# Kernel optimization log

Hardware: AMD Instinct MI355X
Metric: run time of the kernel (lower is better)

Reference implementation:

```python
import jax, jax.numpy as jnp
import numpy as np

NUM_USER = 100000
NUM_ITEM = 50000
N = NUM_USER + NUM_ITEM
E = 1200000
D = 64          # emb_size
F_ITEM = 384    # raw item multimodal feature dim
K = 3           # number of global embedding rows (summed over dim 0)
N_LAYERS = 4
EPS = 1e-8      # F.cosine_similarity default eps


def setup_inputs() -> dict:
    key = jax.random.key(0)
    ks = jax.random.split(key, 9)
    return {
        "adj_row": jax.random.randint(ks[0], (E,), 0, N),
        "adj_col": jax.random.randint(ks[1], (E,), 0, N),
        # scaled like a degree-normalized adjacency (avg degree ~8)
        "adj_val": jax.random.uniform(ks[2], (E,), jnp.float32) / 8.0,
        "user_fea": jax.random.normal(ks[3], (NUM_USER, D), jnp.float32) * 0.1,
        "item_fea": jax.random.normal(ks[4], (NUM_ITEM, F_ITEM), jnp.float32) * 0.1,
        "g_emb_u": jax.random.normal(ks[5], (K, D), jnp.float32) * 0.1,
        "g_emb_i": jax.random.normal(ks[6], (K, D), jnp.float32) * 0.1,
        "mlp_w": jax.random.normal(ks[7], (D, F_ITEM), jnp.float32) * (1.0 / np.sqrt(F_ITEM)),
        "mlp_b": jnp.zeros((D,), jnp.float32),
    }


def _cosine_sim(a, b):
    # matches F.cosine_similarity(a, b, dim=-1) with eps clamp on norms
    na = jnp.maximum(jnp.linalg.norm(a, axis=-1), EPS)
    nb = jnp.maximum(jnp.linalg.norm(b, axis=-1), EPS)
    return jnp.sum(a * b, axis=-1) / (na * nb)


def reference(adj_row, adj_col, adj_val, user_fea, item_fea, g_emb_u, g_emb_i, mlp_w, mlp_b):
    # global embeddings summed over modality dim
    user_emb = user_fea + jnp.sum(g_emb_u, axis=0)                       # [U, D]
    item_emb = jnp.tanh(item_fea @ mlp_w.T + mlp_b) + jnp.sum(g_emb_i, axis=0)  # [I, D]
    ego = jnp.concatenate([user_emb, item_emb], axis=0)                  # [N, D]

    x = ego
    acc = ego  # sum over layers, includes layer-0 (ego) term
    for _ in range(N_LAYERS):
        # sparse adj @ x as gather -> scale -> segment-sum scatter
        x = jax.ops.segment_sum(adj_val[:, None] * x[adj_col], adj_row, num_segments=N)
        w = _cosine_sim(x, ego)     # [N]
        x = w[:, None] * x          # einsum('a,ab->ab')
        acc = acc + x

    return acc[:NUM_USER], acc[NUM_USER:]
```

## Files before the change

kernel.cpp:

```cpp
#include <hip/hip_runtime.h>
#include <hip/hip_bf16.h>

#define U_NUM 100000
#define I_NUM 50000
#define N_NUM 150000
#define E_NUM 1200000
#define D 64
#define F_IT 384
#define CAP 32
#define EPSV 1e-8f
#define FXS 524288.0f
#define FXI (1.0f / 524288.0f)

#define NBIN 586
#define RPB 256
#define FBLK 586
#define CELL_CAP 16
#define OV_CAP 64

typedef unsigned short ushort_t;
typedef unsigned int uint_t;
typedef short bf16x8 __attribute__((ext_vector_type(8)));
typedef float f32x4 __attribute__((ext_vector_type(4)));

__device__ __forceinline__ ushort_t f2bf(float f) {
    uint_t x = __float_as_uint(f);
    uint_t r = x + 0x7fffu + ((x >> 16) & 1u);
    return (ushort_t)(r >> 16);
}
__device__ __forceinline__ float bfu2f(uint_t u_lo16) {
    return __uint_as_float(u_lo16 << 16);
}
__device__ __forceinline__ void dec8(uint4 u, float* f) {
    f[0] = bfu2f(u.x & 0xffffu); f[1] = bfu2f(u.x >> 16);
    f[2] = bfu2f(u.y & 0xffffu); f[3] = bfu2f(u.y >> 16);
    f[4] = bfu2f(u.z & 0xffffu); f[5] = bfu2f(u.z >> 16);
    f[6] = bfu2f(u.w & 0xffffu); f[7] = bfu2f(u.w >> 16);
}

__global__ void k_prep(const float* __restrict__ w, const float* __restrict__ gu,
                       const float* __restrict__ gi,
                       short* __restrict__ wbf, float* __restrict__ gsu,
                       float* __restrict__ gsi, int* __restrict__ ovcnt) {
    int b = blockIdx.x, t = threadIdx.x;
    if (b < 96) {
        int i = b * 256 + t;
        wbf[i] = (short)f2bf(w[i]);
    } else {
        if (t < 64) gsu[t] = gu[t] + gu[64 + t] + gu[128 + t];
        else if (t < 128) { int d = t - 64; gsi[d] = gi[d] + gi[64 + d] + gi[128 + d]; }
        for (int i = t; i < NBIN; i += 256) ovcnt[i] = 0;
    }
}

#define ITEM_B 782
#define USER_B 1563

__global__ __launch_bounds__(256) void k_mega(
        const int* __restrict__ row, const int* __restrict__ col,
        const float* __restrict__ val,
        const float* __restrict__ ufea, const float* __restrict__ ifea,
        const float* __restrict__ bvec,
        const short* __restrict__ wbf,
        const float* __restrict__ gsu, const float* __restrict__ gsi,
        int2* __restrict__ cellbuf, int* __restrict__ cellcnt,
        int* __restrict__ ovcnt, int2* __restrict__ ovbuf,
        float* __restrict__ ego, ushort_t* __restrict__ egob) {
    __shared__ int bincnt[NBIN];
    int b = blockIdx.x;
    int grp = b / 9, slot = b % 9;
    int tid = threadIdx.x;

    if (slot < 2) {
        int fid = grp * 2 + slot;
        if (fid >= FBLK) return;
        for (int i = tid; i < NBIN; i += 256) bincnt[i] = 0;
        __syncthreads();
        int t = fid * 256 + tid;
        if (t < E_NUM / 8) {
#pragma unroll
            for (int k = 0; k < 8; k++) {
                int e = k * (E_NUM / 8) + t;
                int r = row[e], c = col[e];
                float v = val[e];
                int bn = r >> 8;
                int key = c | ((r & 255) << 18);
                int ls = atomicAdd(&bincnt[bn], 1);
                if (ls < CELL_CAP) {
                    cellbuf[((size_t)fid * NBIN + bn) * CELL_CAP + ls] =
                        make_int2(key, __float_as_int(v));
                } else {
                    int o = atomicAdd(&ovcnt[bn], 1);
                    if (o < OV_CAP) ovbuf[bn * OV_CAP + o] = make_int2(key, __float_as_int(v));
                }
            }
        }
        __syncthreads();
        for (int i = tid; i < NBIN; i += 256)
            cellcnt[(size_t)fid * NBIN + i] = min(bincnt[i], CELL_CAP);
    } else if (slot < 4) {
        int iid = grp * 2 + (slot - 2);
        if (iid >= ITEM_B) return;
        int wave = tid >> 6, lane = tid & 63;
        int q = lane >> 4, m = lane & 15;
        int ibase = iid * 64 + wave * 16;
        int irow = min(ibase + m, I_NUM - 1);
        const float* arow = ifea + (size_t)irow * F_IT + q * 8;

        f32x4 av[4];
#pragma unroll
        for (int n = 0; n < 4; n++) av[n] = (f32x4){0.f, 0.f, 0.f, 0.f};
        float4 nfa0 = ((const float4*)(arow))[0];
        float4 nfa1 = ((const float4*)(arow))[1];
#pragma unroll
        for (int c = 0; c < 12; c++) {
            float4 fa0 = nfa0, fa1 = nfa1;
            if (c < 11) {
                nfa0 = ((const float4*)(arow + (c + 1) * 32))[0];
                nfa1 = ((const float4*)(arow + (c + 1) * 32))[1];
            }
            bf16x8 af;
            af[0] = (short)f2bf(fa0.x); af[1] = (short)f2bf(fa0.y);
            af[2] = (short)f2bf(fa0.z); af[3] = (short)f2bf(fa0.w);
            af[4] = (short)f2bf(fa1.x); af[5] = (short)f2bf(fa1.y);
            af[6] = (short)f2bf(fa1.z); af[7] = (short)f2bf(fa1.w);
#pragma unroll
            for (int n = 0; n < 4; n++) {
                bf16x8 bf = *(const bf16x8*)(wbf + (size_t)(n * 16 + m) * F_IT + c * 32 + q * 8);
                av[n] = __builtin_amdgcn_mfma_f32_16x16x32_bf16(af, bf, av[n], 0, 0, 0);
            }
        }
#pragma unroll
        for (int n = 0; n < 4; n++) {
            int dim = n * 16 + m;
            float bb = bvec[dim];
            float gg = gsi[dim];
#pragma unroll
            for (int rr = 0; rr < 4; rr++) {
                int item = ibase + q * 4 + rr;
                if (item < I_NUM) {
                    float v = tanhf(av[n][rr] + bb) + gg;
                    size_t o = (size_t)(U_NUM + item) * D + dim;
                    ego[o] = v;
                    egob[o] = f2bf(v);
                }
            }
        }
    } else {
        int uid = grp * 5 + (slot - 4);
        if (uid >= USER_B) return;
        int t = uid * 256 + tid;
        size_t base = (size_t)t * 16;
        if (base >= (size_t)U_NUM * D) return;
        int d0 = (int)(base & 63);
        float f[16];
#pragma unroll
        for (int k = 0; k < 4; k++) {
            float4 v = ((const float4*)(ufea + base))[k];
            f[4 * k] = v.x; f[4 * k + 1] = v.y; f[4 * k + 2] = v.z; f[4 * k + 3] = v.w;
        }
#pragma unroll
        for (int j = 0; j < 16; j++) f[j] += gsu[d0 + j];
#pragma unroll
        for (int k = 0; k < 4; k++) {
            ((float4*)(ego + base))[k] = make_float4(f[4 * k], f[4 * k + 1], f[4 * k + 2], f[4 * k + 3]);
        }
        uint4 u0, u1;
        u0.x = (uint_t)f2bf(f[0]) | ((uint_t)f2bf(f[1]) << 16);
        u0.y = (uint_t)f2bf(f[2]) | ((uint_t)f2bf(f[3]) << 16);
        u0.z = (uint_t)f2bf(f[4]) | ((uint_t)f2bf(f[5]) << 16);
        u0.w = (uint_t)f2bf(f[6]) | ((uint_t)f2bf(f[7]) << 16);
        u1.x = (uint_t)f2bf(f[8]) | ((uint_t)f2bf(f[9]) << 16);
        u1.y = (uint_t)f2bf(f[10]) | ((uint_t)f2bf(f[11]) << 16);
        u1.z = (uint_t)f2bf(f[12]) | ((uint_t)f2bf(f[13]) << 16);
        u1.w = (uint_t)f2bf(f[14]) | ((uint_t)f2bf(f[15]) << 16);
        ((uint4*)(egob + base))[0] = u0;
        ((uint4*)(egob + base))[1] = u1;
    }
}

__global__ __launch_bounds__(256) void k_bucket(const int2* __restrict__ cellbuf,
                                                const int* __restrict__ cellcnt,
                                                const int* __restrict__ ovcnt,
                                                const int2* __restrict__ ovbuf,
                                                int* __restrict__ cnt,
                                                int2* __restrict__ bkt) {
    __shared__ int lc[RPB];
    int bn = blockIdx.x, tid = threadIdx.x;
    lc[tid] = 0;
    __syncthreads();
    int rbase = bn << 8;
    int f0 = tid, f1 = tid + 256, f2 = tid + 512;
    int c0 = cellcnt[(size_t)f0 * NBIN + bn];
    int c1 = cellcnt[(size_t)f1 * NBIN + bn];
    int c2 = (f2 < FBLK) ? cellcnt[(size_t)f2 * NBIN + bn] : 0;
#pragma unroll
    for (int h = 0; h < 3; h++) {
        int f = (h == 0) ? f0 : ((h == 1) ? f1 : f2);
        int c = (h == 0) ? c0 : ((h == 1) ? c1 : c2);
        const int2* cp = cellbuf + ((size_t)f * NBIN + bn) * CELL_CAP;
        for (int i = 0; i < c; i++) {
            int2 e = cp[i];
            int rl = e.x >> 18;
            int s = atomicAdd(&lc[rl], 1);
            if (s < CAP) bkt[(size_t)(rbase + rl) * CAP + s] = make_int2(e.x & 0x3ffff, e.y);
        }
    }
    int oc = min(ovcnt[bn], OV_CAP);
    for (int i = tid; i < oc; i += 256) {
        int2 e = ovbuf[bn * OV_CAP + i];
        int rl = e.x >> 18;
        int s = atomicAdd(&lc[rl], 1);
        if (s < CAP) bkt[(size_t)(rbase + rl) * CAP + s] = make_int2(e.x & 0x3ffff, e.y);
    }
    __syncthreads();
    int r = rbase + tid;
    if (r < N_NUM) cnt[r] = lc[tid];
}

#define ACC8(A, VS, X) \
    A[0] += __float2int_rn(VS * bfu2f(X.x & 0xffffu)); A[1] += __float2int_rn(VS * bfu2f(X.x >> 16)); \
    A[2] += __float2int_rn(VS * bfu2f(X.y & 0xffffu)); A[3] += __float2int_rn(VS * bfu2f(X.y >> 16)); \
    A[4] += __float2int_rn(VS * bfu2f(X.z & 0xffffu)); A[5] += __float2int_rn(VS * bfu2f(X.z >> 16)); \
    A[6] += __float2int_rn(VS * bfu2f(X.w & 0xffffu)); A[7] += __float2int_rn(VS * bfu2f(X.w >> 16));

__device__ __forceinline__ float row_weight(const float* a, const float* e) {
    float dot = 0.f, nx = 0.f, ne = 0.f;
#pragma unroll
    for (int j = 0; j < 8; j++) {
        dot += a[j] * e[j]; nx += a[j] * a[j]; ne += e[j] * e[j];
    }
#pragma unroll
    for (int m = 1; m < 8; m <<= 1) {
        dot += __shfl_xor(dot, m);
        nx  += __shfl_xor(nx, m);
        ne  += __shfl_xor(ne, m);
    }
    return dot / (fmaxf(sqrtf(nx), EPSV) * fmaxf(sqrtf(ne), EPSV));
}

__device__ __forceinline__ void gather_row(const ushort_t* __restrict__ xb,
                                           const int2* __restrict__ bp, int deg, int l,
                                           int* __restrict__ a) {
#pragma unroll
    for (int j = 0; j < 8; j++) a[j] = 0;
#pragma unroll
    for (int k = 0; k < 4; k++) {
        if (k * 8 < deg) {
            int2 pc = bp[l + k * 8];
            float vs[8];
            uint4 xu[8];
#pragma unroll
            for (int j = 0; j < 8; j++) {
                int cc = __shfl(pc.x, j, 8);
                float v = __int_as_float(__shfl(pc.y, j, 8));
                if ((k * 8 + j) >= deg) { cc = 0; v = 0.f; }
                vs[j] = v * FXS;
                xu[j] = ((const uint4*)xb)[(size_t)cc * 8 + l];
            }
#pragma unroll
            for (int j = 0; j < 8; j++) { ACC8(a, vs[j], xu[j]); }
        }
    }
}

__global__ __launch_bounds__(256) void k_spmm(const ushort_t* __restrict__ xb,
                                              const ushort_t* __restrict__ egob,
                                              const int* __restrict__ cnt,
                                              const int2* __restrict__ bkt,
                                              ushort_t* __restrict__ xob) {
    int t = blockIdx.x * 256 + threadIdx.x;
    int l = t & 7, r = t >> 3;
    if (r >= N_NUM) return;
    int deg = min(cnt[r], CAP);
    int a[8];
    gather_row(xb, bkt + (size_t)r * CAP, deg, l, a);
    float af[8];
#pragma unroll
    for (int j = 0; j < 8; j++) af[j] = (float)a[j] * FXI;
    float e[8]; dec8(((const uint4*)egob)[(size_t)r * 8 + l], e);
    float wgt = row_weight(af, e);
    uint4 ov;
    ov.x = (uint_t)f2bf(wgt * af[0]) | ((uint_t)f2bf(wgt * af[1]) << 16);
    ov.y = (uint_t)f2bf(wgt * af[2]) | ((uint_t)f2bf(wgt * af[3]) << 16);
    ov.z = (uint_t)f2bf(wgt * af[4]) | ((uint_t)f2bf(wgt * af[5]) << 16);
    ov.w = (uint_t)f2bf(wgt * af[6]) | ((uint_t)f2bf(wgt * af[7]) << 16);
    ((uint4*)xob)[(size_t)r * 8 + l] = ov;
}

__global__ __launch_bounds__(256) void k_spmm4(const ushort_t* __restrict__ x3,
                                               const ushort_t* __restrict__ x1,
                                               const ushort_t* __restrict__ x2,
                                               const float* __restrict__ ego,
                                               const int* __restrict__ cnt,
                                               const int2* __restrict__ bkt,
                                               float* __restrict__ out) {
    int t = blockIdx.x * 256 + threadIdx.x;
    int l = t & 7, r = t >> 3;
    if (r >= N_NUM) return;
    int deg = min(cnt[r], CAP);
    int a[8];
    gather_row(x3, bkt + (size_t)r * CAP, deg, l, a);
    float af[8];
#pragma unroll
    for (int j = 0; j < 8; j++) af[j] = (float)a[j] * FXI;
    size_t rb = (size_t)r * D + l * 8;
    float e[8];
    float4 e0 = ((const float4*)(ego + rb))[0];
    float4 e1 = ((const float4*)(ego + rb))[1];
    e[0] = e0.x; e[1] = e0.y; e[2] = e0.z; e[3] = e0.w;
    e[4] = e1.x; e[5] = e1.y; e[6] = e1.z; e[7] = e1.w;
    float wgt = row_weight(af, e);
    float x1d[8], x2d[8], x3d[8];
    dec8(((const uint4*)x1)[(size_t)r * 8 + l], x1d);
    dec8(((const uint4*)x2)[(size_t)r * 8 + l], x2d);
    dec8(((const uint4*)x3)[(size_t)r * 8 + l], x3d);
    float s[8];
#pragma unroll
    for (int j = 0; j < 8; j++) s[j] = e[j] + x1d[j] + x2d[j] + x3d[j] + wgt * af[j];
    ((float4*)(out + rb))[0] = make_float4(s[0], s[1], s[2], s[3]);
    ((float4*)(out + rb))[1] = make_float4(s[4], s[5], s[6], s[7]);
}

extern "C" void kernel_launch(void* const* d_in, const int* in_sizes, int n_in,
                              void* d_out, int out_size, void* d_ws, size_t ws_size,
                              hipStream_t stream) {
    const int*   adj_row  = (const int*)d_in[0];
    const int*   adj_col  = (const int*)d_in[1];
    const float* adj_val  = (const float*)d_in[2];
    const float* user_fea = (const float*)d_in[3];
    const float* item_fea = (const float*)d_in[4];
    const float* gu       = (const float*)d_in[5];
    const float* gi       = (const float*)d_in[6];
    const float* mlp_w    = (const float*)d_in[7];
    const float* mlp_b    = (const float*)d_in[8];

    float* out = (float*)d_out;

    char* ws = (char*)d_ws;
    size_t off = 0;
    float*    ego  = (float*)(ws + off);    off += (size_t)N_NUM * D * 4;
    ushort_t* egob = (ushort_t*)(ws + off); off += (size_t)N_NUM * D * 2;
    size_t x1off = off;
    ushort_t* x1   = (ushort_t*)(ws + off); off += (size_t)N_NUM * D * 2;
    ushort_t* x2   = (ushort_t*)(ws + off); off += (size_t)N_NUM * D * 2;
    ushort_t* x3   = (ushort_t*)(ws + off); off += (size_t)N_NUM * D * 2;
    int*      cnt  = (int*)(ws + off);      off += (size_t)N_NUM * 4;
    short*    wbf  = (short*)(ws + off);    off += (size_t)D * F_IT * 2;
    float*    gsu  = (float*)(ws + off);    off += 64 * 4;
    float*    gsi  = (float*)(ws + off);    off += 64 * 4;
    off = (off + 255) & ~(size_t)255;
    int2*     bkt  = (int2*)(ws + off);     off += (size_t)N_NUM * CAP * 8;
    int*      cellcnt = (int*)(ws + off);   off += (size_t)FBLK * NBIN * 4;
    int*      ovcnt   = (int*)(ws + off);   off += (size_t)NBIN * 4;
    int2*     ovbuf   = (int2*)(ws + off);  off += (size_t)NBIN * OV_CAP * 8;
    int2*     cellbuf = (int2*)(ws + x1off);

    k_prep<<<97, 256, 0, stream>>>(mlp_w, gu, gi, wbf, gsu, gsi, ovcnt);
    k_mega<<<391 * 9, 256, 0, stream>>>(adj_row, adj_col, adj_val, user_fea, item_fea,
                                        mlp_b, wbf, gsu, gsi,
                                        cellbuf, cellcnt, ovcnt, ovbuf, ego, egob);
    k_bucket<<<NBIN, 256, 0, stream>>>(cellbuf, cellcnt, ovcnt, ovbuf, cnt, bkt);
    int g = ((size_t)N_NUM * 8 + 255) / 256;
    k_spmm<<<g, 256, 0, stream>>>(egob, egob, cnt, bkt, x1);
    k_spmm<<<g, 256, 0, stream>>>(x1,   egob, cnt, bkt, x2);
    k_spmm<<<g, 256, 0, stream>>>(x2,   egob, cnt, bkt, x3);
    k_spmm4<<<g, 256, 0, stream>>>(x3, x1, x2, ego, cnt, bkt, out);
}
```

Before: 412.1 us.

## Split mega kernel, use SoA padded adjacency buckets with vector loads

Splits the fused multi-role kernel into separate edge-fill, item-MLP and user-embedding kernels, and doubles the number of fill blocks while halving per-cell capacity. The bucket kernel now writes column indices and values as separate arrays and pads each row to a multiple of 8 with zero entries. The SpMM gather can then read 8 neighbors with int4/float4 loads instead of shuffling, and the SpMM kernels gain occupancy hints. Padding adds wasted gathers of row 0. The smaller cell capacity may push more edges into the bounded overflow buffer, which risks dropping edges if it fills.

New measurement: 442.7 us. +7.4%, slower.

```diff
diff --git a/kernel.cpp b/kernel.cpp
--- a/kernel.cpp
+++ b/kernel.cpp
@@ -14,8 +14,8 @@
 
 #define NBIN 586
 #define RPB 256
-#define FBLK 586
-#define CELL_CAP 16
+#define FBLK 1172
+#define CELL_CAP 8
 #define OV_CAP 64
 
 typedef unsigned short ushort_t;
@@ -53,130 +53,128 @@
     }
 }
 
-#define ITEM_B 782
-#define USER_B 1563
-
-__global__ __launch_bounds__(256) void k_mega(
+__global__ __launch_bounds__(256) void k_fill(
         const int* __restrict__ row, const int* __restrict__ col,
         const float* __restrict__ val,
-        const float* __restrict__ ufea, const float* __restrict__ ifea,
-        const float* __restrict__ bvec,
-        const short* __restrict__ wbf,
-        const float* __restrict__ gsu, const float* __restrict__ gsi,
         int2* __restrict__ cellbuf, int* __restrict__ cellcnt,
-        int* __restrict__ ovcnt, int2* __restrict__ ovbuf,
+        int* __restrict__ ovcnt, int2* __restrict__ ovbuf) {
+    __shared__ int bincnt[NBIN];
+    int fid = blockIdx.x, tid = threadIdx.x;
+    for (int i = tid; i < NBIN; i += 256) bincnt[i] = 0;
+    __syncthreads();
+    int t = fid * 256 + tid;
+    if (t < E_NUM / 4) {
+        int r[4], c[4];
+        float v[4];
+#pragma unroll
+        for (int k = 0; k < 4; k++) {
+            int e = k * (E_NUM / 4) + t;
+            r[k] = row[e]; c[k] = col[e]; v[k] = val[e];
+        }
+#pragma unroll
+        for (int k = 0; k < 4; k++) {
+            int bn = r[k] >> 8;
+            int key = c[k] | ((r[k] & 255) << 18);
+            int ls = atomicAdd(&bincnt[bn], 1);
+            if (ls < CELL_CAP) {
+                cellbuf[((size_t)fid * NBIN + bn) * CELL_CAP + ls] =
+                    make_int2(key, __float_as_int(v[k]));
+            } else {
+                int o = atomicAdd(&ovcnt[bn], 1);
+                if (o < OV_CAP) ovbuf[bn * OV_CAP + o] = make_int2(key, __float_as_int(v[k]));
+            }
+        }
+    }
+    __syncthreads();
+    for (int i = tid; i < NBIN; i += 256)
+        cellcnt[(size_t)fid * NBIN + i] = min(bincnt[i], CELL_CAP);
+}
+
+#define ITEM_B 782
+__global__ __launch_bounds__(256) void k_item(
+        const float* __restrict__ ifea, const float* __restrict__ bvec,
+        const short* __restrict__ wbf, const float* __restrict__ gsi,
         float* __restrict__ ego, ushort_t* __restrict__ egob) {
-    __shared__ int bincnt[NBIN];
-    int b = blockIdx.x;
-    int grp = b / 9, slot = b % 9;
+    int iid = blockIdx.x;
     int tid = threadIdx.x;
-
-    if (slot < 2) {
-        int fid = grp * 2 + slot;
-        if (fid >= FBLK) return;
-        for (int i = tid; i < NBIN; i += 256) bincnt[i] = 0;
-        __syncthreads();
-        int t = fid * 256 + tid;
-        if (t < E_NUM / 8) {
-#pragma unroll
-            for (int k = 0; k < 8; k++) {
-                int e = k * (E_NUM / 8) + t;
-                int r = row[e], c = col[e];
-                float v = val[e];
-                int bn = r >> 8;
-                int key = c | ((r & 255) << 18);
-                int ls = atomicAdd(&bincnt[bn], 1);
-                if (ls < CELL_CAP) {
-                    cellbuf[((size_t)fid * NBIN + bn) * CELL_CAP + ls] =
-                        make_int2(key, __float_as_int(v));
-                } else {
-                    int o = atomicAdd(&ovcnt[bn], 1);
-                    if (o < OV_CAP) ovbuf[bn * OV_CAP + o] = make_int2(key, __float_as_int(v));
-                }
+    int wave = tid >> 6, lane = tid & 63;
+    int q = lane >> 4, m = lane & 15;
+    int ibase = iid * 64 + wave * 16;
+    int irow = min(ibase + m, I_NUM - 1);
+    const float* arow = ifea + (size_t)irow * F_IT + q * 8;
+
+    f32x4 av[4];
+#pragma unroll
+    for (int n = 0; n < 4; n++) av[n] = (f32x4){0.f, 0.f, 0.f, 0.f};
+    float4 nfa0 = ((const float4*)(arow))[0];
+    float4 nfa1 = ((const float4*)(arow))[1];
+#pragma unroll
+    for (int c = 0; c < 12; c++) {
+        float4 fa0 = nfa0, fa1 = nfa1;
+        if (c < 11) {
+            nfa0 = ((const float4*)(arow + (c + 1) * 32))[0];
+            nfa1 = ((const float4*)(arow + (c + 1) * 32))[1];
+        }
+        bf16x8 af;
+        af[0] = (short)f2bf(fa0.x); af[1] = (short)f2bf(fa0.y);
+        af[2] = (short)f2bf(fa0.z); af[3] = (short)f2bf(fa0.w);
+        af[4] = (short)f2bf(fa1.x); af[5] = (short)f2bf(fa1.y);
+        af[6] = (short)f2bf(fa1.z); af[7] = (short)f2bf(fa1.w);
+#pragma unroll
+        for (int n = 0; n < 4; n++) {
+            bf16x8 bf = *(const bf16x8*)(wbf + (size_t)(n * 16 + m) * F_IT + c * 32 + q * 8);
+            av[n] = __builtin_amdgcn_mfma_f32_16x16x32_bf16(af, bf, av[n], 0, 0, 0);
+        }
+    }
+#pragma unroll
+    for (int n = 0; n < 4; n++) {
+        int dim = n * 16 + m;
+        float bb = bvec[dim];
+        float gg = gsi[dim];
+#pragma unroll
+        for (int rr = 0; rr < 4; rr++) {
+            int item = ibase + q * 4 + rr;
+            if (item < I_NUM) {
+                float v = tanhf(av[n][rr] + bb) + gg;
+                size_t o = (size_t)(U_NUM + item) * D + dim;
+                ego[o] = v;
+                egob[o] = f2bf(v);
             }
         }
-        __syncthreads();
-        for (int i = tid; i < NBIN; i += 256)
-            cellcnt[(size_t)fid * NBIN + i] = min(bincnt[i], CELL_CAP);
-    } else if (slot < 4) {
-        int iid = grp * 2 + (slot - 2);
-        if (iid >= ITEM_B) return;
-        int wave = tid >> 6, lane = tid & 63;
-        int q = lane >> 4, m = lane & 15;
-        int ibase = iid * 64 + wave * 16;
-        int irow = min(ibase + m, I_NUM - 1);
-        const float* arow = ifea + (size_t)irow * F_IT + q * 8;
-
-        f32x4 av[4];
-#pragma unroll
-        for (int n = 0; n < 4; n++) av[n] = (f32x4){0.f, 0.f, 0.f, 0.f};
-        float4 nfa0 = ((const float4*)(arow))[0];
-        float4 nfa1 = ((const float4*)(arow))[1];
-#pragma unroll
-        for (int c = 0; c < 12; c++) {
-            float4 fa0 = nfa0, fa1 = nfa1;
-            if (c < 11) {
-                nfa0 = ((const float4*)(arow + (c + 1) * 32))[0];
-                nfa1 = ((const float4*)(arow + (c + 1) * 32))[1];
-            }
-            bf16x8 af;
-            af[0] = (short)f2bf(fa0.x); af[1] = (short)f2bf(fa0.y);
-            af[2] = (short)f2bf(fa0.z); af[3] = (short)f2bf(fa0.w);
-            af[4] = (short)f2bf(fa1.x); af[5] = (short)f2bf(fa1.y);
-            af[6] = (short)f2bf(fa1.z); af[7] = (short)f2bf(fa1.w);
-#pragma unroll
-            for (int n = 0; n < 4; n++) {
-                bf16x8 bf = *(const bf16x8*)(wbf + (size_t)(n * 16 + m) * F_IT + c * 32 + q * 8);
-                av[n] = __builtin_amdgcn_mfma_f32_16x16x32_bf16(af, bf, av[n], 0, 0, 0);
-            }
-        }
-#pragma unroll
-        for (int n = 0; n < 4; n++) {
-            int dim = n * 16 + m;
-            float bb = bvec[dim];
-            float gg = gsi[dim];
-#pragma unroll
-            for (int rr = 0; rr < 4; rr++) {
-                int item = ibase + q * 4 + rr;
-                if (item < I_NUM) {
-                    float v = tanhf(av[n][rr] + bb) + gg;
-                    size_t o = (size_t)(U_NUM + item) * D + dim;
-                    ego[o] = v;
-                    egob[o] = f2bf(v);
-                }
-            }
-        }
-    } else {
-        int uid = grp * 5 + (slot - 4);
-        if (uid >= USER_B) return;
-        int t = uid * 256 + tid;
-        size_t base = (size_t)t * 16;
-        if (base >= (size_t)U_NUM * D) return;
-        int d0 = (int)(base & 63);
-        float f[16];
-#pragma unroll
-        for (int k = 0; k < 4; k++) {
-            float4 v = ((const float4*)(ufea + base))[k];
-            f[4 * k] = v.x; f[4 * k + 1] = v.y; f[4 * k + 2] = v.z; f[4 * k + 3] = v.w;
-        }
-#pragma unroll
-        for (int j = 0; j < 16; j++) f[j] += gsu[d0 + j];
-#pragma unroll
-        for (int k = 0; k < 4; k++) {
-            ((float4*)(ego + base))[k] = make_float4(f[4 * k], f[4 * k + 1], f[4 * k + 2], f[4 * k + 3]);
-        }
-        uint4 u0, u1;
-        u0.x = (uint_t)f2bf(f[0]) | ((uint_t)f2bf(f[1]) << 16);
-        u0.y = (uint_t)f2bf(f[2]) | ((uint_t)f2bf(f[3]) << 16);
-        u0.z = (uint_t)f2bf(f[4]) | ((uint_t)f2bf(f[5]) << 16);
-        u0.w = (uint_t)f2bf(f[6]) | ((uint_t)f2bf(f[7]) << 16);
-        u1.x = (uint_t)f2bf(f[8]) | ((uint_t)f2bf(f[9]) << 16);
-        u1.y = (uint_t)f2bf(f[10]) | ((uint_t)f2bf(f[11]) << 16);
-        u1.z = (uint_t)f2bf(f[12]) | ((uint_t)f2bf(f[13]) << 16);
-        u1.w = (uint_t)f2bf(f[14]) | ((uint_t)f2bf(f[15]) << 16);
-        ((uint4*)(egob + base))[0] = u0;
-        ((uint4*)(egob + base))[1] = u1;
-    }
+    }
+}
+
+#define USER_B 1563
+__global__ __launch_bounds__(256) void k_user(
+        const float* __restrict__ ufea, const float* __restrict__ gsu,
+        float* __restrict__ ego, ushort_t* __restrict__ egob) {
+    int t = blockIdx.x * 256 + threadIdx.x;
+    size_t base = (size_t)t * 16;
+    if (base >= (size_t)U_NUM * D) return;
+    int d0 = (int)(base & 63);
+    float f[16];
+#pragma unroll
+    for (int k = 0; k < 4; k++) {
+        float4 v = ((const float4*)(ufea + base))[k];
+        f[4 * k] = v.x; f[4 * k + 1] = v.y; f[4 * k + 2] = v.z; f[4 * k + 3] = v.w;
+    }
+#pragma unroll
+    for (int j = 0; j < 16; j++) f[j] += gsu[d0 + j];
+#pragma unroll
+    for (int k = 0; k < 4; k++) {
+        ((float4*)(ego + base))[k] = make_float4(f[4 * k], f[4 * k + 1], f[4 * k + 2], f[4 * k + 3]);
+    }
+    uint4 u0, u1;
+    u0.x = (uint_t)f2bf(f[0]) | ((uint_t)f2bf(f[1]) << 16);
+    u0.y = (uint_t)f2bf(f[2]) | ((uint_t)f2bf(f[3]) << 16);
+    u0.z = (uint_t)f2bf(f[4]) | ((uint_t)f2bf(f[5]) << 16);
+    u0.w = (uint_t)f2bf(f[6]) | ((uint_t)f2bf(f[7]) << 16);
+    u1.x = (uint_t)f2bf(f[8]) | ((uint_t)f2bf(f[9]) << 16);
+    u1.y = (uint_t)f2bf(f[10]) | ((uint_t)f2bf(f[11]) << 16);
+    u1.z = (uint_t)f2bf(f[12]) | ((uint_t)f2bf(f[13]) << 16);
+    u1.w = (uint_t)f2bf(f[14]) | ((uint_t)f2bf(f[15]) << 16);
+    ((uint4*)(egob + base))[0] = u0;
+    ((uint4*)(egob + base))[1] = u1;
 }
 
 __global__ __launch_bounds__(256) void k_bucket(const int2* __restrict__ cellbuf,
@@ -184,26 +182,29 @@
                                                 const int* __restrict__ ovcnt,
                                                 const int2* __restrict__ ovbuf,
                                                 int* __restrict__ cnt,
-                                                int2* __restrict__ bkt) {
+                                                int* __restrict__ colsA,
+                                                float* __restrict__ valsA) {
     __shared__ int lc[RPB];
     int bn = blockIdx.x, tid = threadIdx.x;
     lc[tid] = 0;
     __syncthreads();
     int rbase = bn << 8;
-    int f0 = tid, f1 = tid + 256, f2 = tid + 512;
-    int c0 = cellcnt[(size_t)f0 * NBIN + bn];
-    int c1 = cellcnt[(size_t)f1 * NBIN + bn];
-    int c2 = (f2 < FBLK) ? cellcnt[(size_t)f2 * NBIN + bn] : 0;
-#pragma unroll
-    for (int h = 0; h < 3; h++) {
-        int f = (h == 0) ? f0 : ((h == 1) ? f1 : f2);
-        int c = (h == 0) ? c0 : ((h == 1) ? c1 : c2);
-        const int2* cp = cellbuf + ((size_t)f * NBIN + bn) * CELL_CAP;
-        for (int i = 0; i < c; i++) {
-            int2 e = cp[i];
-            int rl = e.x >> 18;
-            int s = atomicAdd(&lc[rl], 1);
-            if (s < CAP) bkt[(size_t)(rbase + rl) * CAP + s] = make_int2(e.x & 0x3ffff, e.y);
+#pragma unroll
+    for (int h = 0; h < 5; h++) {
+        int f = h * 256 + tid;
+        if (f < FBLK) {
+            int c = cellcnt[(size_t)f * NBIN + bn];
+            const int2* cp = cellbuf + ((size_t)f * NBIN + bn) * CELL_CAP;
+            for (int i = 0; i < c; i++) {
+                int2 e = cp[i];
+                int rl = e.x >> 18;
+                int s = atomicAdd(&lc[rl], 1);
+                if (s < CAP) {
+                    size_t o = (size_t)(rbase + rl) * CAP + s;
+                    colsA[o] = e.x & 0x3ffff;
+                    valsA[o] = __int_as_float(e.y);
+                }
+            }
         }
     }
     int oc = min(ovcnt[bn], OV_CAP);
@@ -211,11 +212,24 @@
         int2 e = ovbuf[bn * OV_CAP + i];
         int rl = e.x >> 18;
         int s = atomicAdd(&lc[rl], 1);
-        if (s < CAP) bkt[(size_t)(rbase + rl) * CAP + s] = make_int2(e.x & 0x3ffff, e.y);
+        if (s < CAP) {
+            size_t o = (size_t)(rbase + rl) * CAP + s;
+            colsA[o] = e.x & 0x3ffff;
+            valsA[o] = __int_as_float(e.y);
+        }
     }
     __syncthreads();
     int r = rbase + tid;
-    if (r < N_NUM) cnt[r] = lc[tid];
+    if (r < N_NUM) {
+        int d = min(lc[tid], CAP);
+        int dp = (d + 7) & ~7;
+        for (int s = d; s < dp; s++) {
+            size_t o = (size_t)r * CAP + s;
+            colsA[o] = 0;
+            valsA[o] = 0.f;
+        }
+        cnt[r] = dp;
+    }
 }
 
 #define ACC8(A, VS, X) \
@@ -240,41 +254,49 @@
 }
 
 __device__ __forceinline__ void gather_row(const ushort_t* __restrict__ xb,
-                                           const int2* __restrict__ bp, int deg, int l,
-                                           int* __restrict__ a) {
+                                           const int* __restrict__ colsA,
+                                           const float* __restrict__ valsA,
+                                           int r, int nch, int l, int* __restrict__ a) {
 #pragma unroll
     for (int j = 0; j < 8; j++) a[j] = 0;
+    const int4*   cp = (const int4*)(colsA + (size_t)r * CAP);
+    const float4* vp = (const float4*)(valsA + (size_t)r * CAP);
 #pragma unroll
     for (int k = 0; k < 4; k++) {
-        if (k * 8 < deg) {
-            int2 pc = bp[l + k * 8];
-            float vs[8];
+        if (k < nch) {
+            int4   c03 = cp[2 * k], c47 = cp[2 * k + 1];
+            float4 v03 = vp[2 * k], v47 = vp[2 * k + 1];
             uint4 xu[8];
-#pragma unroll
-            for (int j = 0; j < 8; j++) {
-                int cc = __shfl(pc.x, j, 8);
-                float v = __int_as_float(__shfl(pc.y, j, 8));
-                if ((k * 8 + j) >= deg) { cc = 0; v = 0.f; }
-                vs[j] = v * FXS;
-                xu[j] = ((const uint4*)xb)[(size_t)cc * 8 + l];
-            }
-#pragma unroll
-            for (int j = 0; j < 8; j++) { ACC8(a, vs[j], xu[j]); }
-        }
-    }
-}
-
-__global__ __launch_bounds__(256) void k_spmm(const ushort_t* __restrict__ xb,
-                                              const ushort_t* __restrict__ egob,
-                                              const int* __restrict__ cnt,
-                                              const int2* __restrict__ bkt,
-                                              ushort_t* __restrict__ xob) {
+            xu[0] = ((const uint4*)xb)[(size_t)c03.x * 8 + l];
+            xu[1] = ((const uint4*)xb)[(size_t)c03.y * 8 + l];
+            xu[2] = ((const uint4*)xb)[(size_t)c03.z * 8 + l];
+            xu[3] = ((const uint4*)xb)[(size_t)c03.w * 8 + l];
+            xu[4] = ((const uint4*)xb)[(size_t)c47.x * 8 + l];
+            xu[5] = ((const uint4*)xb)[(size_t)c47.y * 8 + l];
+            xu[6] = ((const uint4*)xb)[(size_t)c47.z * 8 + l];
+            xu[7] = ((const uint4*)xb)[(size_t)c47.w * 8 + l];
+            float vs0 = v03.x * FXS, vs1 = v03.y * FXS, vs2 = v03.z * FXS, vs3 = v03.w * FXS;
+            float vs4 = v47.x * FXS, vs5 = v47.y * FXS, vs6 = v47.z * FXS, vs7 = v47.w * FXS;
+            ACC8(a, vs0, xu[0]); ACC8(a, vs1, xu[1]);
+            ACC8(a, vs2, xu[2]); ACC8(a, vs3, xu[3]);
+            ACC8(a, vs4, xu[4]); ACC8(a, vs5, xu[5]);
+            ACC8(a, vs6, xu[6]); ACC8(a, vs7, xu[7]);
+        }
+    }
+}
+
+__device__ __forceinline__ void spmm_body(const ushort_t* __restrict__ xb,
+                                          const ushort_t* __restrict__ egob,
+                                          const int* __restrict__ cnt,
+                                          const int* __restrict__ colsA,
+                                          const float* __restrict__ valsA,
+                                          ushort_t* __restrict__ xob) {
     int t = blockIdx.x * 256 + threadIdx.x;
     int l = t & 7, r = t >> 3;
     if (r >= N_NUM) return;
-    int deg = min(cnt[r], CAP);
+    int nch = cnt[r] >> 3;
     int a[8];
-    gather_row(xb, bkt + (size_t)r * CAP, deg, l, a);
+    gather_row(xb, colsA, valsA, r, nch, l, a);
     float af[8];
 #pragma unroll
     for (int j = 0; j < 8; j++) af[j] = (float)a[j] * FXI;
@@ -288,19 +310,35 @@
     ((uint4*)xob)[(size_t)r * 8 + l] = ov;
 }
 
-__global__ __launch_bounds__(256) void k_spmm4(const ushort_t* __restrict__ x3,
-                                               const ushort_t* __restrict__ x1,
-                                               const ushort_t* __restrict__ x2,
-                                               const float* __restrict__ ego,
-                                               const int* __restrict__ cnt,
-                                               const int2* __restrict__ bkt,
-                                               float* __restrict__ out) {
+__global__ __launch_bounds__(256, 5) void k_spmmA(const ushort_t* __restrict__ xb,
+        const ushort_t* __restrict__ egob, const int* __restrict__ cnt,
+        const int* __restrict__ colsA, const float* __restrict__ valsA,
+        ushort_t* __restrict__ xob) { spmm_body(xb, egob, cnt, colsA, valsA, xob); }
+
+__global__ __launch_bounds__(256, 5) void k_spmmB(const ushort_t* __restrict__ xb,
+        const ushort_t* __restrict__ egob, const int* __restrict__ cnt,
+        const int* __restrict__ colsA, const float* __restrict__ valsA,
+        ushort_t* __restrict__ xob) { spmm_body(xb, egob, cnt, colsA, valsA, xob); }
+
+__global__ __launch_bounds__(256, 5) void k_spmmC(const ushort_t* __restrict__ xb,
+        const ushort_t* __restrict__ egob, const int* __restrict__ cnt,
+        const int* __restrict__ colsA, const float* __restrict__ valsA,
+        ushort_t* __restrict__ xob) { spmm_body(xb, egob, cnt, colsA, valsA, xob); }
+
+__global__ __launch_bounds__(256, 5) void k_spmm4(const ushort_t* __restrict__ x3,
+                                                  const ushort_t* __restrict__ x1,
+                                                  const ushort_t* __restrict__ x2,
+                                                  const float* __restrict__ ego,
+                                                  const int* __restrict__ cnt,
+                                                  const int* __restrict__ colsA,
+                                                  const float* __restrict__ valsA,
+                                                  float* __restrict__ out) {
     int t = blockIdx.x * 256 + threadIdx.x;
     int l = t & 7, r = t >> 3;
     if (r >= N_NUM) return;
-    int deg = min(cnt[r], CAP);
+    int nch = cnt[r] >> 3;
     int a[8];
-    gather_row(x3, bkt + (size_t)r * CAP, deg, l, a);
+    gather_row(x3, colsA, valsA, r, nch, l, a);
     float af[8];
 #pragma unroll
     for (int j = 0; j < 8; j++) af[j] = (float)a[j] * FXI;
@@ -350,20 +388,23 @@
     float*    gsu  = (float*)(ws + off);    off += 64 * 4;
     float*    gsi  = (float*)(ws + off);    off += 64 * 4;
     off = (off + 255) & ~(size_t)255;
-    int2*     bkt  = (int2*)(ws + off);     off += (size_t)N_NUM * CAP * 8;
+    int*      colsA = (int*)(ws + off);     off += (size_t)N_NUM * CAP * 4;
+    float*    valsA = (float*)(ws + off);   off += (size_t)N_NUM * CAP * 4;
     int*      cellcnt = (int*)(ws + off);   off += (size_t)FBLK * NBIN * 4;
     int*      ovcnt   = (int*)(ws + off);   off += (size_t)NBIN * 4;
     int2*     ovbuf   = (int2*)(ws + off);  off += (size_t)NBIN * OV_CAP * 8;
     int2*     cellbuf = (int2*)(ws + x1off);
 
     k_prep<<<97, 256, 0, stream>>>(mlp_w, gu, gi, wbf, gsu, gsi, ovcnt);
-    k_mega<<<391 * 9, 256, 0, stream>>>(adj_row, adj_col, adj_val, user_fea, item_fea,
-                                        mlp_b, wbf, gsu, gsi,
-                                        cellbuf, cellcnt, ovcnt, ovbuf, ego, egob);
-    k_bucket<<<NBIN, 256, 0, stream>>>(cellbuf, cellcnt, ovcnt, ovbuf, cnt, bkt);
+    k_fill<<<FBLK, 256, 0, stream>>>(adj_row, adj_col, adj_val,
+                                     cellbuf, cellcnt, ovcnt, ovbuf);
+    k_item<<<ITEM_B, 256, 0, stream>>>(item_fea, mlp_b, wbf, gsi, ego, egob);
+    k_user<<<USER_B, 256, 0, stream>>>(user_fea, gsu, ego, egob);
+    k_bucket<<<NBIN, 256, 0, stream>>>(cellbuf, cellcnt, ovcnt, ovbuf,
+                                       cnt, colsA, valsA);
     int g = ((size_t)N_NUM * 8 + 255) / 256;
-    k_spmm<<<g, 256, 0, stream>>>(egob, egob, cnt, bkt, x1);
-    k_spmm<<<g, 256, 0, stream>>>(x1,   egob, cnt, bkt, x2);
-    k_spmm<<<g, 256, 0, stream>>>(x2,   egob, cnt, bkt, x3);
-    k_spmm4<<<g, 256, 0, stream>>>(x3, x1, x2, ego, cnt, bkt, out);
-}
+    k_spmmA<<<g, 256, 0, stream>>>(egob, egob, cnt, colsA, valsA, x1);
+    k_spmmB<<<g, 256, 0, stream>>>(x1,   egob, cnt, colsA, valsA, x2);
+    k_spmmC<<<g, 256, 0, stream>>>(x2,   egob, cnt, colsA, valsA, x3);
+    k_spmm4<<<g, 256, 0, stream>>>(x3, x1, x2, ego, cnt, colsA, valsA, out);
+}
```
